# Optimization experiments

Hardware: AMD Instinct MI355X
Metric: run time of the kernel (lower is better)

The kernel has to match this reference:

```python
import jax, jax.numpy as jnp
import numpy as np

T, B, D = 1024, 64, 1024  # time steps, batch, num_inputs == num_hiddens
SIGMA = 0.01


def setup_inputs() -> dict:
    key = jax.random.key(0)
    ks = jax.random.split(key, 7)
    w = lambda k: (jax.random.normal(k, (D, D), dtype=jnp.float32) * SIGMA)
    return {
        "inputs": jax.random.normal(ks[0], (T, B, D), dtype=jnp.float32),
        "W_xz": w(ks[1]), "W_hz": w(ks[2]), "b_z": jnp.zeros((D,), jnp.float32),
        "W_xr": w(ks[3]), "W_hr": w(ks[4]), "b_r": jnp.zeros((D,), jnp.float32),
        "W_xh": w(ks[5]), "W_hh": w(ks[6]), "b_h": jnp.zeros((D,), jnp.float32),
    }


def reference(inputs, W_xz, W_hz, b_z, W_xr, W_hr, b_r, W_xh, W_hh, b_h):
    # Precompute all input-to-hidden projections in batched GEMMs (T*B rows).
    Xz = jnp.einsum('tbi,ih->tbh', inputs, W_xz) + b_z
    Xr = jnp.einsum('tbi,ih->tbh', inputs, W_xr) + b_r
    Xh = jnp.einsum('tbi,ih->tbh', inputs, W_xh) + b_h

    def step(H, xs):
        xz, xr, xh = xs
        Z = jax.nn.sigmoid(xz + H @ W_hz)
        R = jax.nn.sigmoid(xr + H @ W_hr)
        # torch precedence: R * H @ W_hh == R * (H @ W_hh)
        H_tilde = jnp.tanh(xh + R * (H @ W_hh))
        H_new = Z * H + (1.0 - Z) * H_tilde
        return H_new, H_new

    H0 = jnp.zeros((inputs.shape[1], inputs.shape[2]), dtype=inputs.dtype)
    H_last, outputs = jax.lax.scan(step, H0, (Xz, Xr, Xh))
    return outputs, H_last
```

## Files before the change

kernel.cpp:

```cpp
#include <hip/hip_runtime.h>
#include <hip/hip_bf16.h>
#include <stdint.h>

typedef unsigned int u32;
typedef unsigned short u16;
typedef short bf16x8 __attribute__((ext_vector_type(8)));
typedef float f32x4 __attribute__((ext_vector_type(4)));
typedef u32 u32x4 __attribute__((ext_vector_type(4)));

#define T_STEPS 1024
#define BATCH   64
#define DIM     1024
#define NGRP    8
#define GWG     32
#define NTHR    512
#define SENT    0xFFFFFFFFu

__device__ __forceinline__ u16 f2bf(float f) {
  u32 u = __float_as_uint(f);
  return (u16)((u + 0x7FFFu + ((u >> 16) & 1u)) >> 16);
}
__device__ __forceinline__ float sigm(float x) { return 1.0f / (1.0f + __expf(-x)); }
__device__ __forceinline__ float tanh_f(float x) {
  x = fminf(8.0f, fmaxf(-8.0f, x));
  float e = __expf(2.0f * x);
  return (e - 1.0f) / (e + 1.0f);
}

__global__ void gru_pack3(const float* __restrict__ Wz, const float* __restrict__ Wr,
                          const float* __restrict__ Wh, u16* __restrict__ wp) {
  int idx = blockIdx.x * 256 + threadIdx.x;
  if (idx >= GWG * 8 * 2 * 3 * 4 * 64) return;
  int lane = idx & 63; int r = idx >> 6;
  int ks = r & 3; r >>= 2;
  int n = r % 3; r /= 3;
  int cg = r & 1; r >>= 1;
  int wv = r & 7; int wid = r >> 3;
  int k0 = wv * 128 + ks * 32 + (lane >> 4) * 8;
  int col = wid * 32 + cg * 16 + (lane & 15);
  const float* W = (n == 0) ? Wz : (n == 1) ? Wr : Wh;
  u16* dst = wp + (size_t)idx * 8;
#pragma unroll
  for (int j = 0; j < 8; ++j) dst[j] = f2bf(W[(size_t)(k0 + j) * DIM + col]);
}

#define WAIT0 asm volatile("s_waitcnt vmcnt(0)" ::: "memory"); __builtin_amdgcn_sched_barrier(0)
#define MFMA_(A, B, C) __builtin_amdgcn_mfma_f32_16x16x32_bf16(__builtin_bit_cast(bf16x8, A), B, C, 0, 0, 0)
#define PK2(a, b) ((((u32)f2bf(b)) << 16) | (u32)f2bf(a))

__launch_bounds__(NTHR, 2)
__global__ void gru_scan(const float* __restrict__ inputs,
                         const float* __restrict__ bz, const float* __restrict__ br,
                         const float* __restrict__ bh,
                         const u16* __restrict__ wpackH, const u16* __restrict__ wpackX,
                         u32* hhist, float* __restrict__ out) {
  __shared__ float part[8][2][4][64][6];

  const int tid = threadIdx.x;
  const int g   = blockIdx.x >> 5;
  const int wid = blockIdx.x & 31;
  const int wv = tid >> 6;
  const int lane = tid & 63;

  bf16x8 bregH[2][3][4], bregX[2][3][4];
  {
    const u16* wph = wpackH + (size_t)(wid * 8 + wv) * (2 * 3 * 4 * 512);
    const u16* wpx = wpackX + (size_t)(wid * 8 + wv) * (2 * 3 * 4 * 512);
#pragma unroll
    for (int cg = 0; cg < 2; ++cg)
#pragma unroll
      for (int n = 0; n < 3; ++n)
#pragma unroll
        for (int ks = 0; ks < 4; ++ks) {
          const int off = (((cg * 3 + n) * 4 + ks) * 512) + lane * 8;
          bregH[cg][n][ks] = *(const bf16x8*)(wph + off);
          asm volatile("" : "+v"(bregH[cg][n][ks]));
          bregX[cg][n][ks] = *(const bf16x8*)(wpx + off);
          asm volatile("" : "+v"(bregX[cg][n][ks]));
        }
  }

  const int grow = tid >> 4;
  const int cp = tid & 15;
  const int cgg = cp >> 3;
  const int c16 = 2 * (cp & 7);
  const int col0 = wid * 32 + cgg * 16 + c16;
  const float b_z0 = bz[col0], b_z1 = bz[col0 + 1];
  const float b_r0 = br[col0], b_r1 = br[col0 + 1];
  const float b_h0 = bh[col0], b_h1 = bh[col0 + 1];
  const int cell0 = (grow >> 2) * 16 + c16;
  const int wrd = grow & 3;
  float hp0 = 0.f, hp1 = 0.f;

  f32x4 xc[2][3];
#define COMPX(ts) { \
  u32x4 xa0, xa1, xa2, xa3; \
  const float* xb_ = inputs + (size_t)(ts) * (BATCH * DIM) \
                   + (size_t)(8 * g + (lane & 7)) * DIM + wv * 128 + (lane >> 4) * 8; \
  { f32x4 lo, hi; \
    lo = *(const f32x4*)(xb_ + 0);  hi = *(const f32x4*)(xb_ + 4); \
    xa0[0]=PK2(lo[0],lo[1]); xa0[1]=PK2(lo[2],lo[3]); xa0[2]=PK2(hi[0],hi[1]); xa0[3]=PK2(hi[2],hi[3]); \
    lo = *(const f32x4*)(xb_ + 32); hi = *(const f32x4*)(xb_ + 36); \
    xa1[0]=PK2(lo[0],lo[1]); xa1[1]=PK2(lo[2],lo[3]); xa1[2]=PK2(hi[0],hi[1]); xa1[3]=PK2(hi[2],hi[3]); \
    lo = *(const f32x4*)(xb_ + 64); hi = *(const f32x4*)(xb_ + 68); \
    xa2[0]=PK2(lo[0],lo[1]); xa2[1]=PK2(lo[2],lo[3]); xa2[2]=PK2(hi[0],hi[1]); xa2[3]=PK2(hi[2],hi[3]); \
    lo = *(const f32x4*)(xb_ + 96); hi = *(const f32x4*)(xb_ + 100); \
    xa3[0]=PK2(lo[0],lo[1]); xa3[1]=PK2(lo[2],lo[3]); xa3[2]=PK2(hi[0],hi[1]); xa3[3]=PK2(hi[2],hi[3]); } \
  if ((lane & 15) >= 8) { xa0 = (u32x4){0,0,0,0}; xa1 = (u32x4){0,0,0,0}; \
                          xa2 = (u32x4){0,0,0,0}; xa3 = (u32x4){0,0,0,0}; } \
  _Pragma("unroll") for (int cg_ = 0; cg_ < 2; ++cg_) \
  _Pragma("unroll") for (int n_ = 0; n_ < 3; ++n_) { \
    f32x4 a_ = (f32x4){0.f, 0.f, 0.f, 0.f}; \
    a_ = MFMA_(xa0, bregX[cg_][n_][0], a_); \
    a_ = MFMA_(xa1, bregX[cg_][n_][1], a_); \
    a_ = MFMA_(xa2, bregX[cg_][n_][2], a_); \
    a_ = MFMA_(xa3, bregX[cg_][n_][3], a_); \
    xc[cg_][n_] = a_; } }

  COMPX(0);

#pragma unroll 1
  for (int t = 0; t < T_STEPS; ++t) {
    f32x4 vz[2], vr[2], vhh[2];
#pragma unroll
    for (int cg = 0; cg < 2; ++cg) {
      vz[cg] = xc[cg][0]; vr[cg] = xc[cg][1]; vhh[cg] = (f32x4){0.f, 0.f, 0.f, 0.f};
    }

    if (t > 0) {
      const u32* hb = hhist + ((size_t)(t - 1) * NGRP + g) * 4096
                    + (size_t)(lane & 7) * 512 + wv * 64 + (lane >> 4) * 4;
      u32x4 ha0, ha1, ha2, ha3;
      for (;;) {
        asm volatile("global_load_dwordx4 %0, %1, off sc0 sc1" : "=v"(ha0) : "v"(hb));
        asm volatile("global_load_dwordx4 %0, %1, off offset:64 sc0 sc1" : "=v"(ha1) : "v"(hb));
        asm volatile("global_load_dwordx4 %0, %1, off offset:128 sc0 sc1" : "=v"(ha2) : "v"(hb));
        asm volatile("global_load_dwordx4 %0, %1, off offset:192 sc0 sc1" : "=v"(ha3) : "v"(hb));
        WAIT0;
        u32 bad = (u32)(ha0[0] == SENT) | (u32)(ha0[1] == SENT)
                | (u32)(ha0[2] == SENT) | (u32)(ha0[3] == SENT)
                | (u32)(ha1[0] == SENT) | (u32)(ha1[1] == SENT)
                | (u32)(ha1[2] == SENT) | (u32)(ha1[3] == SENT)
                | (u32)(ha2[0] == SENT) | (u32)(ha2[1] == SENT)
                | (u32)(ha2[2] == SENT) | (u32)(ha2[3] == SENT)
                | (u32)(ha3[0] == SENT) | (u32)(ha3[1] == SENT)
                | (u32)(ha3[2] == SENT) | (u32)(ha3[3] == SENT);
        if (__all((int)(bad == 0))) break;
        __builtin_amdgcn_s_sleep(1);
      }
      asm volatile("" ::: "memory");
      if ((lane & 15) >= 8) { ha0 = (u32x4){0,0,0,0}; ha1 = (u32x4){0,0,0,0};
                              ha2 = (u32x4){0,0,0,0}; ha3 = (u32x4){0,0,0,0}; }
#pragma unroll
      for (int cg = 0; cg < 2; ++cg) {
        vz[cg] = MFMA_(ha0, bregH[cg][0][0], vz[cg]);
        vz[cg] = MFMA_(ha1, bregH[cg][0][1], vz[cg]);
        vz[cg] = MFMA_(ha2, bregH[cg][0][2], vz[cg]);
        vz[cg] = MFMA_(ha3, bregH[cg][0][3], vz[cg]);
        vr[cg] = MFMA_(ha0, bregH[cg][1][0], vr[cg]);
        vr[cg] = MFMA_(ha1, bregH[cg][1][1], vr[cg]);
        vr[cg] = MFMA_(ha2, bregH[cg][1][2], vr[cg]);
        vr[cg] = MFMA_(ha3, bregH[cg][1][3], vr[cg]);
        vhh[cg] = MFMA_(ha0, bregH[cg][2][0], vhh[cg]);
        vhh[cg] = MFMA_(ha1, bregH[cg][2][1], vhh[cg]);
        vhh[cg] = MFMA_(ha2, bregH[cg][2][2], vhh[cg]);
        vhh[cg] = MFMA_(ha3, bregH[cg][2][3], vhh[cg]);
      }
    }

#pragma unroll
    for (int cg = 0; cg < 2; ++cg) {
      *(float2*)&part[wv][cg][0][lane][0] = make_float2(vz[cg][0], vz[cg][1]);
      *(float2*)&part[wv][cg][0][lane][2] = make_float2(vz[cg][2], vz[cg][3]);
      *(float2*)&part[wv][cg][1][lane][0] = make_float2(vr[cg][0], vr[cg][1]);
      *(float2*)&part[wv][cg][1][lane][2] = make_float2(vr[cg][2], vr[cg][3]);
      *(float2*)&part[wv][cg][2][lane][0] = make_float2(xc[cg][2][0], xc[cg][2][1]);
      *(float2*)&part[wv][cg][2][lane][2] = make_float2(xc[cg][2][2], xc[cg][2][3]);
      *(float2*)&part[wv][cg][3][lane][0] = make_float2(vhh[cg][0], vhh[cg][1]);
      *(float2*)&part[wv][cg][3][lane][2] = make_float2(vhh[cg][2], vhh[cg][3]);
    }
    __syncthreads();

    float hn0 = 0.f, hn1 = 0.f;
    if (tid < 128) {
      float sz0 = 0, sz1 = 0, sr0 = 0, sr1 = 0, sx0 = 0, sx1 = 0, sh0 = 0, sh1 = 0;
#pragma unroll
      for (int w = 0; w < 8; ++w) {
        sz0 += part[w][cgg][0][cell0][wrd];     sz1 += part[w][cgg][0][cell0 + 1][wrd];
        sr0 += part[w][cgg][1][cell0][wrd];     sr1 += part[w][cgg][1][cell0 + 1][wrd];
        sx0 += part[w][cgg][2][cell0][wrd];     sx1 += part[w][cgg][2][cell0 + 1][wrd];
        sh0 += part[w][cgg][3][cell0][wrd];     sh1 += part[w][cgg][3][cell0 + 1][wrd];
      }
      float z0 = sigm(sz0 + b_z0), z1 = sigm(sz1 + b_z1);
      float r0 = sigm(sr0 + b_r0), r1 = sigm(sr1 + b_r1);
      float th0 = tanh_f(sx0 + b_h0 + r0 * sh0);
      float th1 = tanh_f(sx1 + b_h1 + r1 * sh1);
      hn0 = z0 * hp0 + (1.f - z0) * th0;
      hn1 = z1 * hp1 + (1.f - z1) * th1;
      hp0 = hn0; hp1 = hn1;
      u32 pk = ((u32)f2bf(hn1) << 16) | f2bf(hn0);
      u32* hpw = hhist + ((size_t)t * NGRP + g) * 4096 + (size_t)grow * 512 + wid * 16 + cp;
      asm volatile("global_store_dword %0, %1, off sc0 sc1" :: "v"(hpw), "v"(pk) : "memory");
    }
    __syncthreads();

    if (tid < 128) {
      float* op = out + (size_t)t * (BATCH * DIM) + (size_t)(8 * g + grow) * DIM + col0;
      *(float2*)op = make_float2(hn0, hn1);
      if (t == T_STEPS - 1) {
        float* fo = out + (size_t)T_STEPS * (BATCH * DIM) + (size_t)(8 * g + grow) * DIM + col0;
        *(float2*)fo = make_float2(hn0, hn1);
      }
    }
    if (t + 1 < T_STEPS) COMPX(t + 1);
  }
#undef COMPX
}

extern "C" void kernel_launch(void* const* d_in, const int* in_sizes, int n_in,
                              void* d_out, int out_size, void* d_ws, size_t ws_size,
                              hipStream_t stream) {
  const float* inputs = (const float*)d_in[0];
  const float* Wxz = (const float*)d_in[1];
  const float* Whz = (const float*)d_in[2];
  const float* bz  = (const float*)d_in[3];
  const float* Wxr = (const float*)d_in[4];
  const float* Whr = (const float*)d_in[5];
  const float* br  = (const float*)d_in[6];
  const float* Wxh = (const float*)d_in[7];
  const float* Whh = (const float*)d_in[8];
  const float* bh  = (const float*)d_in[9];
  float* out = (float*)d_out;

  char* ws = (char*)d_ws;
  u32* hhist  = (u32*)ws;
  size_t hhist_bytes = (size_t)T_STEPS * NGRP * 4096 * 4;
  u16* wpackH = (u16*)(ws + hhist_bytes);
  u16* wpackX = (u16*)(ws + hhist_bytes + 6291456);
  size_t need = hhist_bytes + 2 * 6291456;
  if (ws_size < need) return;

  hipMemsetAsync(hhist, 0xFF, hhist_bytes, stream);

  const int pk = GWG * 8 * 2 * 3 * 4 * 64;
  hipLaunchKernelGGL(gru_pack3, dim3((pk + 255) / 256), dim3(256), 0, stream,
                     Whz, Whr, Whh, wpackH);
  hipLaunchKernelGGL(gru_pack3, dim3((pk + 255) / 256), dim3(256), 0, stream,
                     Wxz, Wxr, Wxh, wpackX);
  hipLaunchKernelGGL(gru_scan, dim3(NGRP * GWG), dim3(NTHR), 0, stream,
                     inputs, bz, br, bh, wpackH, wpackX, hhist, out);
}
```

Measured before the change: 7.553 ms.

## Remap workgroups to XCDs so recurrent exchange stays in local L2

Each workgroup reads its hardware XCC id and takes a ticket at startup. If every XCD holds exactly 32 blocks, batch group g is reassigned to match the XCD. The h-history stores and polling loads then drop the sc1 (system-coherent) bit and go through the shared per-XCD L2. A fallback path keeps the original fully coherent loads and stores, and after many spins the poll alternates to coherent loads. The aim is to remove cross-die coherence latency from the per-step dependency chain, at the cost of an extra init kernel, a grid-wide startup barrier, and reliance on XCC placement.

```diff
diff --git a/kernel.cpp b/kernel.cpp
--- a/kernel.cpp
+++ b/kernel.cpp
@@ -16,6 +16,11 @@
 #define NTHR    512
 #define SENT    0xFFFFFFFFu
 
+#define CTL_XCNT(x)   ((x)*16)
+#define CTL_ARR       128
+#define CTL_MODE      144
+#define CTL_U32       256
+
 __device__ __forceinline__ u16 f2bf(float f) {
   u32 u = __float_as_uint(f);
   return (u16)((u + 0x7FFFu + ((u >> 16) & 1u)) >> 16);
@@ -25,6 +30,10 @@
   x = fminf(8.0f, fmaxf(-8.0f, x));
   float e = __expf(2.0f * x);
   return (e - 1.0f) / (e + 1.0f);
+}
+
+__global__ void gru_init(u32* ctrl) {
+  if (threadIdx.x < CTL_U32) ctrl[threadIdx.x] = 0;
 }
 
 __global__ void gru_pack3(const float* __restrict__ Wz, const float* __restrict__ Wr,
@@ -48,17 +57,14 @@
 #define MFMA_(A, B, C) __builtin_amdgcn_mfma_f32_16x16x32_bf16(__builtin_bit_cast(bf16x8, A), B, C, 0, 0, 0)
 #define PK2(a, b) ((((u32)f2bf(b)) << 16) | (u32)f2bf(a))
 
-__launch_bounds__(NTHR, 2)
-__global__ void gru_scan(const float* __restrict__ inputs,
-                         const float* __restrict__ bz, const float* __restrict__ br,
-                         const float* __restrict__ bh,
-                         const u16* __restrict__ wpackH, const u16* __restrict__ wpackX,
-                         u32* hhist, float* __restrict__ out) {
-  __shared__ float part[8][2][4][64][6];
-
+template <int MODE>
+__device__ __forceinline__ void scan_run(
+    int g, int wid, const float* __restrict__ inputs,
+    const float* __restrict__ bz, const float* __restrict__ br, const float* __restrict__ bh,
+    const u16* __restrict__ wpackH, const u16* __restrict__ wpackX,
+    u32* hhist, float* __restrict__ out,
+    float (&part)[8][2][4][64][6]) {
   const int tid = threadIdx.x;
-  const int g   = blockIdx.x >> 5;
-  const int wid = blockIdx.x & 31;
   const int wv = tid >> 6;
   const int lane = tid & 63;
 
@@ -131,11 +137,20 @@
       const u32* hb = hhist + ((size_t)(t - 1) * NGRP + g) * 4096
                     + (size_t)(lane & 7) * 512 + wv * 64 + (lane >> 4) * 4;
       u32x4 ha0, ha1, ha2, ha3;
+      u32 spins = 0;
       for (;;) {
-        asm volatile("global_load_dwordx4 %0, %1, off sc0 sc1" : "=v"(ha0) : "v"(hb));
-        asm volatile("global_load_dwordx4 %0, %1, off offset:64 sc0 sc1" : "=v"(ha1) : "v"(hb));
-        asm volatile("global_load_dwordx4 %0, %1, off offset:128 sc0 sc1" : "=v"(ha2) : "v"(hb));
-        asm volatile("global_load_dwordx4 %0, %1, off offset:192 sc0 sc1" : "=v"(ha3) : "v"(hb));
+        bool ic = (MODE == 2) || (spins > 4096u && (spins & 1u));
+        if (ic) {
+          asm volatile("global_load_dwordx4 %0, %1, off sc0 sc1" : "=v"(ha0) : "v"(hb));
+          asm volatile("global_load_dwordx4 %0, %1, off offset:64 sc0 sc1" : "=v"(ha1) : "v"(hb));
+          asm volatile("global_load_dwordx4 %0, %1, off offset:128 sc0 sc1" : "=v"(ha2) : "v"(hb));
+          asm volatile("global_load_dwordx4 %0, %1, off offset:192 sc0 sc1" : "=v"(ha3) : "v"(hb));
+        } else {
+          asm volatile("global_load_dwordx4 %0, %1, off sc0" : "=v"(ha0) : "v"(hb));
+          asm volatile("global_load_dwordx4 %0, %1, off offset:64 sc0" : "=v"(ha1) : "v"(hb));
+          asm volatile("global_load_dwordx4 %0, %1, off offset:128 sc0" : "=v"(ha2) : "v"(hb));
+          asm volatile("global_load_dwordx4 %0, %1, off offset:192 sc0" : "=v"(ha3) : "v"(hb));
+        }
         WAIT0;
         u32 bad = (u32)(ha0[0] == SENT) | (u32)(ha0[1] == SENT)
                 | (u32)(ha0[2] == SENT) | (u32)(ha0[3] == SENT)
@@ -146,6 +161,7 @@
                 | (u32)(ha3[0] == SENT) | (u32)(ha3[1] == SENT)
                 | (u32)(ha3[2] == SENT) | (u32)(ha3[3] == SENT);
         if (__all((int)(bad == 0))) break;
+        ++spins;
         __builtin_amdgcn_s_sleep(1);
       }
       asm volatile("" ::: "memory");
@@ -200,7 +216,10 @@
       hp0 = hn0; hp1 = hn1;
       u32 pk = ((u32)f2bf(hn1) << 16) | f2bf(hn0);
       u32* hpw = hhist + ((size_t)t * NGRP + g) * 4096 + (size_t)grow * 512 + wid * 16 + cp;
-      asm volatile("global_store_dword %0, %1, off sc0 sc1" :: "v"(hpw), "v"(pk) : "memory");
+      if (MODE == 1)
+        asm volatile("global_store_dword %0, %1, off sc0" :: "v"(hpw), "v"(pk) : "memory");
+      else
+        asm volatile("global_store_dword %0, %1, off sc0 sc1" :: "v"(hpw), "v"(pk) : "memory");
     }
     __syncthreads();
 
@@ -215,6 +234,53 @@
     if (t + 1 < T_STEPS) COMPX(t + 1);
   }
 #undef COMPX
+}
+
+__launch_bounds__(NTHR, 2)
+__global__ void gru_scan(const float* __restrict__ inputs,
+                         const float* __restrict__ bz, const float* __restrict__ br,
+                         const float* __restrict__ bh,
+                         const u16* __restrict__ wpackH, const u16* __restrict__ wpackX,
+                         u32* hhist, u32* ctrl, float* __restrict__ out) {
+  __shared__ float part[8][2][4][64][6];
+  __shared__ u32 meta[4];
+
+  if (threadIdx.x == 0) {
+    u32 x;
+    asm volatile("s_getreg_b32 %0, hwreg(HW_REG_XCC_ID)" : "=s"(x));
+    x &= 7;
+    u32 tk = __hip_atomic_fetch_add(ctrl + CTL_XCNT(x), 1u,
+                                    __ATOMIC_RELAXED, __HIP_MEMORY_SCOPE_AGENT);
+    __hip_atomic_fetch_add(ctrl + CTL_ARR, 1u, __ATOMIC_RELEASE, __HIP_MEMORY_SCOPE_AGENT);
+    while (__hip_atomic_load(ctrl + CTL_ARR, __ATOMIC_ACQUIRE, __HIP_MEMORY_SCOPE_AGENT)
+           < (u32)(NGRP * GWG))
+      __builtin_amdgcn_s_sleep(4);
+    if (blockIdx.x == 0) {
+      u32 uni = 1;
+      for (int i = 0; i < 8; ++i)
+        if (__hip_atomic_load(ctrl + CTL_XCNT(i), __ATOMIC_RELAXED,
+                              __HIP_MEMORY_SCOPE_AGENT) != GWG) uni = 0;
+      __hip_atomic_store(ctrl + CTL_MODE, uni ? 1u : 2u,
+                         __ATOMIC_RELEASE, __HIP_MEMORY_SCOPE_AGENT);
+    }
+    u32 m;
+    for (;;) {
+      m = __hip_atomic_load(ctrl + CTL_MODE, __ATOMIC_ACQUIRE, __HIP_MEMORY_SCOPE_AGENT);
+      if (m != 0) break;
+      __builtin_amdgcn_s_sleep(4);
+    }
+    meta[0] = m;
+    meta[1] = (m == 1) ? x : (blockIdx.x >> 5);
+    meta[2] = (m == 1) ? tk : (blockIdx.x & 31);
+  }
+  __syncthreads();
+  const u32 m = meta[0];
+  const int g = (int)meta[1];
+  const int wid = (int)meta[2];
+  if (m == 1 && wid >= GWG) return;
+
+  if (m == 1) scan_run<1>(g, wid, inputs, bz, br, bh, wpackH, wpackX, hhist, out, part);
+  else        scan_run<2>(g, wid, inputs, bz, br, bh, wpackH, wpackX, hhist, out, part);
 }
 
 extern "C" void kernel_launch(void* const* d_in, const int* in_sizes, int n_in,
@@ -233,20 +299,22 @@
   float* out = (float*)d_out;
 
   char* ws = (char*)d_ws;
-  u32* hhist  = (u32*)ws;
+  u32* ctrl = (u32*)ws;
+  u32* hhist = (u32*)(ws + 32768);
   size_t hhist_bytes = (size_t)T_STEPS * NGRP * 4096 * 4;
-  u16* wpackH = (u16*)(ws + hhist_bytes);
-  u16* wpackX = (u16*)(ws + hhist_bytes + 6291456);
-  size_t need = hhist_bytes + 2 * 6291456;
+  u16* wpackH = (u16*)(ws + 32768 + hhist_bytes);
+  u16* wpackX = (u16*)(ws + 32768 + hhist_bytes + 6291456);
+  size_t need = 32768 + hhist_bytes + 2 * 6291456;
   if (ws_size < need) return;
 
   hipMemsetAsync(hhist, 0xFF, hhist_bytes, stream);
 
+  hipLaunchKernelGGL(gru_init, dim3(1), dim3(256), 0, stream, ctrl);
   const int pk = GWG * 8 * 2 * 3 * 4 * 64;
   hipLaunchKernelGGL(gru_pack3, dim3((pk + 255) / 256), dim3(256), 0, stream,
                      Whz, Whr, Whh, wpackH);
   hipLaunchKernelGGL(gru_pack3, dim3((pk + 255) / 256), dim3(256), 0, stream,
                      Wxz, Wxr, Wxh, wpackX);
   hipLaunchKernelGGL(gru_scan, dim3(NGRP * GWG), dim3(NTHR), 0, stream,
-                     inputs, bz, br, bh, wpackH, wpackX, hhist, out);
-}
+                     inputs, bz, br, bh, wpackH, wpackX, hhist, ctrl, out);
+}
```

Result: no change. 7.660 ms (+1.4%).
